# Kernel tuning notes

Hardware: AMD Instinct MI355X
Metric: run time of the kernel (lower is better)

## Reference

```python
import jax, jax.numpy as jnp
import numpy as np

N_NODES = 100_000
N_EDGES = 1_600_000
IN_FEAT = 128
N_HEADS = 8
OUT_FEAT = 16
HF = N_HEADS * OUT_FEAT  # 128
NEG_SLOPE = 0.2


def setup_inputs() -> dict:
    key = jax.random.key(0)
    k = jax.random.split(key, 9)
    x = jax.random.normal(k[0], (N_NODES, IN_FEAT), dtype=jnp.float32)
    src = jax.random.randint(k[1], (N_EDGES,), 0, N_NODES, dtype=jnp.int64)
    dst = jax.random.randint(k[2], (N_EDGES,), 0, N_NODES, dtype=jnp.int64)
    sv = 1.0 / np.sqrt(IN_FEAT)
    sa = 1.0 / np.sqrt(HF)
    Wv = jax.random.normal(k[3], (IN_FEAT, HF), dtype=jnp.float32) * sv
    bv = jnp.zeros((HF,), dtype=jnp.float32)
    Wq = jax.random.normal(k[4], (HF, N_HEADS), dtype=jnp.float32) * sa
    bq = jnp.zeros((N_HEADS,), dtype=jnp.float32)
    Wk = jax.random.normal(k[5], (HF, N_HEADS), dtype=jnp.float32) * sa
    bk = jnp.zeros((N_HEADS,), dtype=jnp.float32)
    return {"x": x, "src": src, "dst": dst, "Wv": Wv, "bv": bv,
            "Wq": Wq, "bq": bq, "Wk": Wk, "bk": bk}


def reference(x, src, dst, Wv, bv, Wq, bq, Wk, bk):
    # Dense projections (homogeneous graph: h_src == h_dst == h)
    h = x @ Wv + bv                       # [N, H*F]
    q = h @ Wq + bq                       # [N, H]  (query, attached via dst)
    k = h @ Wk + bk                       # [N, H]  (key, attached via src)
    u = h.reshape(N_NODES, N_HEADS, OUT_FEAT)  # [N, H, F]

    # Edge scores: u_add_v('k','q') -> e_ij = k[src] + q[dst], then leaky-relu
    e = k[src] + q[dst]                   # [E, H]
    coeff = jnp.where(e >= 0, e, NEG_SLOPE * e)

    # Segment softmax over incoming edges of each destination node
    seg_max = jax.ops.segment_max(coeff, dst, num_segments=N_NODES)   # [N, H]
    ex = jnp.exp(coeff - seg_max[dst])                                # [E, H]
    denom = jax.ops.segment_sum(ex, dst, num_segments=N_NODES)       # [N, H]
    attn = ex / denom[dst]                                           # [E, H]

    # Weighted message + scatter-sum aggregate
    m = u[src] * attn[:, :, None]                                    # [E, H, F]
    v = jax.ops.segment_sum(m, dst, num_segments=N_NODES)            # [N, H, F]

    return jnp.mean(v, axis=1)                                       # [N, F]
```

## Files before the change

kernel.cpp:

```cpp
#include <hip/hip_runtime.h>
#include <hip/hip_fp16.h>

#define NFEAT 128
#define NHEADS 8
#define OUTF 16
#define NPB 256
#define MAXNB 512
#define CAP 4736

typedef _Float16 half8 __attribute__((ext_vector_type(8)));
typedef float float4v __attribute__((ext_vector_type(4)));

__global__ __launch_bounds__(256) void prep_kernel(
    const float* __restrict__ Wv, const float* __restrict__ bv,
    const float* __restrict__ Wq, const float* __restrict__ bq,
    const float* __restrict__ Wk, const float* __restrict__ bk,
    float* __restrict__ Wvq, float* __restrict__ Wvk,
    float* __restrict__ bq2, float* __restrict__ bk2, int* __restrict__ tail)
{
    const int t = threadIdx.x;
    const int idx = blockIdx.x * 256 + t;
    if (idx < MAXNB) tail[idx] = 0;
    const int m  = idx >> 10;
    const int j  = (idx >> 3) & 127;
    const int hd = idx & 7;
    const float* w = m ? Wk : Wq;
    float acc = 0.f;
#pragma unroll 8
    for (int c = 0; c < NFEAT; c++) acc += Wv[j * NFEAT + c] * w[c * NHEADS + hd];
    if (m) Wvk[j * NHEADS + hd] = acc;
    else   Wvq[j * NHEADS + hd] = acc;

    if (blockIdx.x == 0 && t < 16) {
        int mm = t >> 3, hh = t & 7;
        const float* ww = mm ? Wk : Wq;
        float a = mm ? bk[hh] : bq[hh];
        for (int c = 0; c < NFEAT; c++) a += bv[c] * ww[c * NHEADS + hh];
        if (mm) bk2[hh] = a;
        else    bq2[hh] = a;
    }
}

__global__ __launch_bounds__(256) void k1_kernel(
    const float* __restrict__ x, const float* __restrict__ Wv,
    const float* __restrict__ bv, const float* __restrict__ Wvq,
    const float* __restrict__ Wvk, const float* __restrict__ bq2,
    const float* __restrict__ bk2, __half* __restrict__ h,
    float* __restrict__ qarr, float* __restrict__ karr, int M,
    const int* __restrict__ src, const int* __restrict__ dst,
    int* __restrict__ tail, int* __restrict__ bin, int E, int NB,
    int GB, int BB)
{
    __shared__ char smem[144 * 136 * 2];
    const int bid = blockIdx.x;
    const int t = threadIdx.x;

    if ((bid & 1) == 0) {
        const int gb = bid >> 1;
        if (gb >= GB) return;
        _Float16 (*sw)[136] = (_Float16(*)[136])smem;

        for (int i = t; i < 128 * 128; i += 256) {
            int k = i >> 7, n = i & 127;
            sw[n][k] = (_Float16)Wv[i];
        }
        for (int i = t; i < 128 * 16; i += 256) {
            int k = i >> 4, o = i & 15;
            float v = (o < 8) ? Wvq[k * 8 + o] : Wvk[k * 8 + (o - 8)];
            sw[128 + o][k] = (_Float16)v;
        }
        __syncthreads();

        const int wave = t >> 6, lane = t & 63;
        const int quad = lane >> 4, l16 = lane & 15;
        const int nstrips = (M + 15) >> 4;

        float bvv[8];
#pragma unroll
        for (int tl = 0; tl < 8; tl++) bvv[tl] = bv[tl * 16 + l16];
        const float qb = (l16 < 8) ? bq2[l16] : bk2[l16 - 8];

#pragma unroll
        for (int s = 0; s < 4; s++) {
            const int strip = gb * 16 + wave * 4 + s;
            if (strip >= nstrips) break;
            const int row0 = strip * 16;
            const int xr = row0 + l16;
            const bool ok = (xr < M);
            const float* xp = x + (size_t)xr * NFEAT + quad * 8;

            half8 af[4];
#pragma unroll
            for (int kc = 0; kc < 4; kc++) {
                float4 f0 = make_float4(0.f, 0.f, 0.f, 0.f);
                float4 f1 = make_float4(0.f, 0.f, 0.f, 0.f);
                if (ok) {
                    f0 = *(const float4*)(xp + kc * 32);
                    f1 = *(const float4*)(xp + kc * 32 + 4);
                }
                half8 a;
                a[0] = (_Float16)f0.x; a[1] = (_Float16)f0.y;
                a[2] = (_Float16)f0.z; a[3] = (_Float16)f0.w;
                a[4] = (_Float16)f1.x; a[5] = (_Float16)f1.y;
                a[6] = (_Float16)f1.z; a[7] = (_Float16)f1.w;
                af[kc] = a;
            }

            float4v acc[9];
#pragma unroll
            for (int tl = 0; tl < 9; tl++) acc[tl] = (float4v){0.f, 0.f, 0.f, 0.f};

#pragma unroll
            for (int kc = 0; kc < 4; kc++) {
#pragma unroll
                for (int tl = 0; tl < 9; tl++) {
                    half8 b = *(const half8*)&sw[tl * 16 + l16][kc * 32 + quad * 8];
                    acc[tl] = __builtin_amdgcn_mfma_f32_16x16x32_f16(af[kc], b, acc[tl], 0, 0, 0);
                }
            }

#pragma unroll
            for (int r = 0; r < 4; r++) {
                int row = row0 + quad * 4 + r;
                if (row < M) {
#pragma unroll
                    for (int tl = 0; tl < 8; tl++)
                        h[(size_t)row * NFEAT + tl * 16 + l16] =
                            __float2half(acc[tl][r] + bvv[tl]);
                    float qv = acc[8][r] + qb;
                    if (l16 < 8) qarr[(size_t)row * NHEADS + l16] = qv;
                    else         karr[(size_t)row * NHEADS + (l16 - 8)] = qv;
                }
            }
        }
    } else {
        const int bb = bid >> 1;
        if (bb >= BB) return;
        int* lcnt  = (int*)smem;
        int* lbase = lcnt + MAXNB;
        const int e0 = bb * 4096;

        for (int i = t; i < MAXNB; i += 256) lcnt[i] = 0;
        __syncthreads();

        int pack[16], bkt[16], rank[16];
#pragma unroll
        for (int k = 0; k < 16; k++) {
            int e = e0 + k * 256 + t;
            bkt[k] = -1;
            if (e < E) {
                int d = dst[e];
                pack[k] = (src[e] << 8) | (d & (NPB - 1));
                bkt[k]  = d >> 8;
                rank[k] = atomicAdd(&lcnt[bkt[k]], 1);
            }
        }
        __syncthreads();
        for (int i = t; i < NB; i += 256)
            lbase[i] = lcnt[i] ? atomicAdd(&tail[i], lcnt[i]) : 0;
        __syncthreads();

#pragma unroll
        for (int k = 0; k < 16; k++) {
            if (bkt[k] >= 0) {
                int pos = lbase[bkt[k]] + rank[k];
                if (pos < CAP) bin[(size_t)bkt[k] * CAP + pos] = pack[k];
            }
        }
    }
}

__global__ __launch_bounds__(512) void bucket_build_kernel(
    const int* __restrict__ bin, const int* __restrict__ tail,
    int* __restrict__ deg, int* __restrict__ off,
    int* __restrict__ csr, int N, int NB)
{
    __shared__ int stail[MAXNB];
    __shared__ int lcnt[NPB];
    __shared__ int lcur[NPB];
    __shared__ int lcsr[CAP];

    const int b = blockIdx.x;
    const int t = threadIdx.x;

    stail[t] = (t < NB) ? tail[t] : 0;
    if (t < NPB) lcnt[t] = 0;
    __syncthreads();

    for (int o = 1; o < MAXNB; o <<= 1) {
        int u = (t >= o) ? stail[t - o] : 0;
        __syncthreads();
        stail[t] += u;
        __syncthreads();
    }
    const int gbase = (b > 0) ? stail[b - 1] : 0;
    const int cnt = min(stail[b] - gbase, CAP);
    const int n0 = b << 8;
    const int* mybin = bin + (size_t)b * CAP;

    for (int i = t; i < cnt; i += 512) atomicAdd(&lcnt[mybin[i] & (NPB - 1)], 1);
    __syncthreads();

    if (t < NPB) lcur[t] = lcnt[t];
    __syncthreads();
    for (int o = 1; o < NPB; o <<= 1) {
        int u = (t < NPB && t >= o) ? lcur[t - o] : 0;
        __syncthreads();
        if (t < NPB) lcur[t] += u;
        __syncthreads();
    }
    if (t < NPB) {
        int excl = lcur[t] - lcnt[t];
        lcur[t] = excl;
        int node = n0 + t;
        if (node < N) {
            deg[node] = lcnt[t];
            off[node] = gbase + excl;
        }
    }
    __syncthreads();

    for (int i = t; i < cnt; i += 512) {
        int p = mybin[i];
        int r = atomicAdd(&lcur[p & (NPB - 1)], 1);
        lcsr[r] = p >> 8;
    }
    __syncthreads();

    for (int i = t; i < cnt; i += 512) csr[gbase + i] = lcsr[i];
}

__global__ __launch_bounds__(256) void agg_kernel(
    const int* __restrict__ csr, const int* __restrict__ off,
    const int* __restrict__ deg, const float* __restrict__ karr,
    const float* __restrict__ qarr, const __half* __restrict__ h,
    float* __restrict__ out, int nnodes)
{
    const int wave = threadIdx.x >> 6;
    const int lane = threadIdx.x & 63;
    const int d = blockIdx.x * 4 + wave;
    if (d >= nnodes) return;

    const int dg = deg[d];
    const int o0 = off[d];
    const int h8  = lane & 7;
    const int eg  = lane >> 4;
    const int l16 = lane & 15;
    const int hd  = l16 >> 1;
    const float q1 = qarr[d * NHEADS + h8];
    const __half* hbase = h + l16 * 8;

    __half2 acc0 = __float2half2_rn(0.f);
    __half2 acc1 = __float2half2_rn(0.f);
    __half2 acc2 = __float2half2_rn(0.f);
    __half2 acc3 = __float2half2_rn(0.f);
    float den8 = 0.f;

    for (int c0 = 0; c0 < dg; c0 += 64) {
        const int cnt = min(64, dg - c0);
        int sv = (lane < cnt) ? csr[o0 + c0 + lane] : 0;
        for (int g0 = 0; g0 < cnt; g0 += 8) {
            const int epos = g0 + (lane >> 3);
            int s8 = __shfl(sv, epos, 64);
            float p = 0.f;
            if (epos < cnt) {
                float c = karr[s8 * NHEADS + h8] + q1;
                c = fmaxf(c, 0.2f * c);
                p = __expf(c) * 0.0009765625f;
            }
            den8 += p;
            __half2 ph2 = __half2half2(__float2half(p));
            int phi = *(int*)&ph2;
#pragma unroll
            for (int i = 0; i < 2; ++i) {
                int jr  = (i << 2) + eg;
                int sl  = __shfl(sv, g0 + jr, 64);
                int pw  = __shfl(phi, (jr << 3) + hd, 64);
                __half2 pv = *(__half2*)&pw;
                float4 raw = *(const float4*)(hbase + (size_t)sl * NFEAT);
                __half2 v0 = *(__half2*)&raw.x;
                __half2 v1 = *(__half2*)&raw.y;
                __half2 v2 = *(__half2*)&raw.z;
                __half2 v3 = *(__half2*)&raw.w;
                acc0 = __hfma2(pv, v0, acc0);
                acc1 = __hfma2(pv, v1, acc1);
                acc2 = __hfma2(pv, v2, acc2);
                acc3 = __hfma2(pv, v3, acc3);
            }
        }
    }

    den8 += __shfl_xor(den8, 8, 64);
    den8 += __shfl_xor(den8, 16, 64);
    den8 += __shfl_xor(den8, 32, 64);
    float dh = __shfl(den8, hd, 64);

    float f[8];
    f[0] = __low2float(acc0); f[1] = __high2float(acc0);
    f[2] = __low2float(acc1); f[3] = __high2float(acc1);
    f[4] = __low2float(acc2); f[5] = __high2float(acc2);
    f[6] = __low2float(acc3); f[7] = __high2float(acc3);

#pragma unroll
    for (int o = 16; o <= 32; o <<= 1)
#pragma unroll
        for (int i = 0; i < 8; i++) f[i] += __shfl_xor(f[i], o, 64);

    const float inv = (dg > 0) ? 0.125f / dh : 0.f;
#pragma unroll
    for (int i = 0; i < 8; i++) f[i] *= inv;

#pragma unroll
    for (int o = 2; o <= 8; o <<= 1)
#pragma unroll
        for (int i = 0; i < 8; i++) f[i] += __shfl_xor(f[i], o, 64);

    if (lane < 2) {
        float4* o4 = (float4*)(out + (size_t)d * OUTF + lane * 8);
        o4[0] = make_float4(f[0], f[1], f[2], f[3]);
        o4[1] = make_float4(f[4], f[5], f[6], f[7]);
    }
}

extern "C" void kernel_launch(void* const* d_in, const int* in_sizes, int n_in,
                              void* d_out, int out_size, void* d_ws, size_t ws_size,
                              hipStream_t stream)
{
    const float* x   = (const float*)d_in[0];
    const int*   src = (const int*)d_in[1];
    const int*   dst = (const int*)d_in[2];
    const float* Wv  = (const float*)d_in[3];
    const float* bv  = (const float*)d_in[4];
    const float* Wq  = (const float*)d_in[5];
    const float* bq  = (const float*)d_in[6];
    const float* Wk  = (const float*)d_in[7];
    const float* bk  = (const float*)d_in[8];
    float* out = (float*)d_out;

    const int N = in_sizes[0] / NFEAT;
    const int E = in_sizes[1];
    const int NB = (N + NPB - 1) / NPB;

    __half* h   = (__half*)d_ws;
    float* qarr = (float*)d_ws + (size_t)N * (NFEAT / 2);
    float* karr = qarr + (size_t)N * NHEADS;
    int* deg    = (int*)(karr + (size_t)N * NHEADS);
    int* off    = deg + N;
    int* csr    = off + N;
    float* Wvq  = (float*)(csr + E);
    float* Wvk  = Wvq + NFEAT * NHEADS;
    float* bq2  = Wvk + NFEAT * NHEADS;
    float* bk2  = bq2 + NHEADS;
    int* tail   = (int*)(bk2 + NHEADS);
    int* bin    = tail + MAXNB;

    prep_kernel<<<dim3(8), dim3(256), 0, stream>>>(Wv, bv, Wq, bq, Wk, bk,
                                                   Wvq, Wvk, bq2, bk2, tail);

    const int nstrips = (N + 15) / 16;
    const int GB = (nstrips + 15) / 16;
    const int BB = (E + 4095) / 4096;
    const int grid1 = 2 * max(GB, BB);
    k1_kernel<<<dim3(grid1), dim3(256), 0, stream>>>(
        x, Wv, bv, Wvq, Wvk, bq2, bk2, h, qarr, karr, N,
        src, dst, tail, bin, E, NB, GB, BB);

    bucket_build_kernel<<<dim3(NB), dim3(512), 0, stream>>>(
        bin, tail, deg, off, csr, N, NB);

    agg_kernel<<<dim3((N + 3) / 4), dim3(256), 0, stream>>>(
        csr, off, deg, karr, qarr, h, out, N);
}
```

Baseline: 242.9 us.

## Fuse CSR bucket build into aggregation and restructure projection GEMM per-wave

Merges the bucket-build and aggregation kernels so each block sorts its bucket of edges into shared memory and aggregates its 128 destination nodes directly. This drops the global CSR, degree and offset arrays and one launch. Buckets shrink to 128 nodes with a smaller cap. The projection GEMM now keeps each wave's weight column slice in registers, with 9 waves per 576-thread block streaming 18 strips through shared memory. The fused kernel has only 8 waves per bucket, which risks load imbalance and lower occupancy in aggregation, and the cap risks silently dropping edges if a bucket overflows.

```diff
diff --git a/kernel.cpp b/kernel.cpp
--- a/kernel.cpp
+++ b/kernel.cpp
@@ -4,9 +4,10 @@
 #define NFEAT 128
 #define NHEADS 8
 #define OUTF 16
-#define NPB 256
-#define MAXNB 512
-#define CAP 4736
+#define NPB 128
+#define MAXNB 1024
+#define CAP 2816
+#define SPB 18
 
 typedef _Float16 half8 __attribute__((ext_vector_type(8)));
 typedef float float4v __attribute__((ext_vector_type(4)));
@@ -41,7 +42,7 @@
     }
 }
 
-__global__ __launch_bounds__(256) void k1_kernel(
+__global__ __launch_bounds__(576) void k1_kernel(
     const float* __restrict__ x, const float* __restrict__ Wv,
     const float* __restrict__ bv, const float* __restrict__ Wvq,
     const float* __restrict__ Wvk, const float* __restrict__ bq2,
@@ -51,117 +52,113 @@
     int* __restrict__ tail, int* __restrict__ bin, int E, int NB,
     int GB, int BB)
 {
-    __shared__ char smem[144 * 136 * 2];
+    __shared__ alignas(16) int smem4[2048];
     const int bid = blockIdx.x;
     const int t = threadIdx.x;
 
     if ((bid & 1) == 0) {
         const int gb = bid >> 1;
         if (gb >= GB) return;
-        _Float16 (*sw)[136] = (_Float16(*)[136])smem;
-
-        for (int i = t; i < 128 * 128; i += 256) {
-            int k = i >> 7, n = i & 127;
-            sw[n][k] = (_Float16)Wv[i];
-        }
-        for (int i = t; i < 128 * 16; i += 256) {
-            int k = i >> 4, o = i & 15;
-            float v = (o < 8) ? Wvq[k * 8 + o] : Wvk[k * 8 + (o - 8)];
-            sw[128 + o][k] = (_Float16)v;
-        }
-        __syncthreads();
-
-        const int wave = t >> 6, lane = t & 63;
+        _Float16 (*sa)[136] = (_Float16(*)[136])smem4;
+
+        const int wave = t / 64, lane = t & 63;
         const int quad = lane >> 4, l16 = lane & 15;
         const int nstrips = (M + 15) >> 4;
 
-        float bvv[8];
-#pragma unroll
-        for (int tl = 0; tl < 8; tl++) bvv[tl] = bv[tl * 16 + l16];
-        const float qb = (l16 < 8) ? bq2[l16] : bk2[l16 - 8];
-
-#pragma unroll
-        for (int s = 0; s < 4; s++) {
-            const int strip = gb * 16 + wave * 4 + s;
+        half8 bf[4];
+        float bias;
+        if (wave < 8) {
+            const int n = wave * 16 + l16;
+#pragma unroll
+            for (int kc = 0; kc < 4; kc++) {
+                half8 b;
+#pragma unroll
+                for (int j = 0; j < 8; j++)
+                    b[j] = (_Float16)Wv[(kc * 32 + quad * 8 + j) * NFEAT + n];
+                bf[kc] = b;
+            }
+            bias = bv[wave * 16 + l16];
+        } else {
+            const int o = l16;
+#pragma unroll
+            for (int kc = 0; kc < 4; kc++) {
+                half8 b;
+#pragma unroll
+                for (int j = 0; j < 8; j++) {
+                    int k = kc * 32 + quad * 8 + j;
+                    b[j] = (_Float16)((o < 8) ? Wvq[k * 8 + o] : Wvk[k * 8 + (o - 8)]);
+                }
+                bf[kc] = b;
+            }
+            bias = (o < 8) ? bq2[o] : bk2[o - 8];
+        }
+
+        for (int s = 0; s < SPB; s++) {
+            const int strip = gb * SPB + s;
             if (strip >= nstrips) break;
             const int row0 = strip * 16;
-            const int xr = row0 + l16;
-            const bool ok = (xr < M);
-            const float* xp = x + (size_t)xr * NFEAT + quad * 8;
-
-            half8 af[4];
+
+            __syncthreads();
+            if (t < 512) {
+                int r = t >> 5, c4 = (t & 31) << 2;
+                int row = row0 + r;
+                float4 v = make_float4(0.f, 0.f, 0.f, 0.f);
+                if (row < M) v = *(const float4*)&x[(size_t)row * NFEAT + c4];
+                sa[r][c4 + 0] = (_Float16)v.x; sa[r][c4 + 1] = (_Float16)v.y;
+                sa[r][c4 + 2] = (_Float16)v.z; sa[r][c4 + 3] = (_Float16)v.w;
+            }
+            __syncthreads();
+
+            float4v acc = (float4v){0.f, 0.f, 0.f, 0.f};
 #pragma unroll
             for (int kc = 0; kc < 4; kc++) {
-                float4 f0 = make_float4(0.f, 0.f, 0.f, 0.f);
-                float4 f1 = make_float4(0.f, 0.f, 0.f, 0.f);
-                if (ok) {
-                    f0 = *(const float4*)(xp + kc * 32);
-                    f1 = *(const float4*)(xp + kc * 32 + 4);
-                }
-                half8 a;
-                a[0] = (_Float16)f0.x; a[1] = (_Float16)f0.y;
-                a[2] = (_Float16)f0.z; a[3] = (_Float16)f0.w;
-                a[4] = (_Float16)f1.x; a[5] = (_Float16)f1.y;
-                a[6] = (_Float16)f1.z; a[7] = (_Float16)f1.w;
-                af[kc] = a;
-            }
-
-            float4v acc[9];
-#pragma unroll
-            for (int tl = 0; tl < 9; tl++) acc[tl] = (float4v){0.f, 0.f, 0.f, 0.f};
-
-#pragma unroll
-            for (int kc = 0; kc < 4; kc++) {
-#pragma unroll
-                for (int tl = 0; tl < 9; tl++) {
-                    half8 b = *(const half8*)&sw[tl * 16 + l16][kc * 32 + quad * 8];
-                    acc[tl] = __builtin_amdgcn_mfma_f32_16x16x32_f16(af[kc], b, acc[tl], 0, 0, 0);
-                }
+                half8 a = *(const half8*)&sa[l16][kc * 32 + quad * 8];
+                acc = __builtin_amdgcn_mfma_f32_16x16x32_f16(a, bf[kc], acc, 0, 0, 0);
             }
 
 #pragma unroll
             for (int r = 0; r < 4; r++) {
                 int row = row0 + quad * 4 + r;
                 if (row < M) {
-#pragma unroll
-                    for (int tl = 0; tl < 8; tl++)
-                        h[(size_t)row * NFEAT + tl * 16 + l16] =
-                            __float2half(acc[tl][r] + bvv[tl]);
-                    float qv = acc[8][r] + qb;
-                    if (l16 < 8) qarr[(size_t)row * NHEADS + l16] = qv;
-                    else         karr[(size_t)row * NHEADS + (l16 - 8)] = qv;
+                    float v = acc[r] + bias;
+                    if (wave < 8)
+                        h[(size_t)row * NFEAT + wave * 16 + l16] = __float2half(v);
+                    else if (l16 < 8)
+                        qarr[(size_t)row * NHEADS + l16] = v;
+                    else
+                        karr[(size_t)row * NHEADS + (l16 - 8)] = v;
                 }
             }
         }
     } else {
         const int bb = bid >> 1;
         if (bb >= BB) return;
-        int* lcnt  = (int*)smem;
-        int* lbase = lcnt + MAXNB;
-        const int e0 = bb * 4096;
-
-        for (int i = t; i < MAXNB; i += 256) lcnt[i] = 0;
-        __syncthreads();
-
-        int pack[16], bkt[16], rank[16];
-#pragma unroll
-        for (int k = 0; k < 16; k++) {
-            int e = e0 + k * 256 + t;
+        int* lcnt  = smem4;
+        int* lbase = smem4 + MAXNB;
+        const int e0 = bb * 4608;
+
+        for (int i = t; i < MAXNB; i += 576) lcnt[i] = 0;
+        __syncthreads();
+
+        int pack[8], bkt[8], rank[8];
+#pragma unroll
+        for (int k = 0; k < 8; k++) {
+            int e = e0 + k * 576 + t;
             bkt[k] = -1;
             if (e < E) {
                 int d = dst[e];
-                pack[k] = (src[e] << 8) | (d & (NPB - 1));
-                bkt[k]  = d >> 8;
+                pack[k] = (src[e] << 7) | (d & (NPB - 1));
+                bkt[k]  = d >> 7;
                 rank[k] = atomicAdd(&lcnt[bkt[k]], 1);
             }
         }
         __syncthreads();
-        for (int i = t; i < NB; i += 256)
+        for (int i = t; i < NB; i += 576)
             lbase[i] = lcnt[i] ? atomicAdd(&tail[i], lcnt[i]) : 0;
         __syncthreads();
 
 #pragma unroll
-        for (int k = 0; k < 16; k++) {
+        for (int k = 0; k < 8; k++) {
             if (bkt[k] >= 0) {
                 int pos = lbase[bkt[k]] + rank[k];
                 if (pos < CAP) bin[(size_t)bkt[k] * CAP + pos] = pack[k];
@@ -170,33 +167,24 @@
     }
 }
 
-__global__ __launch_bounds__(512) void bucket_build_kernel(
+__global__ __launch_bounds__(512) void buildagg_kernel(
     const int* __restrict__ bin, const int* __restrict__ tail,
-    int* __restrict__ deg, int* __restrict__ off,
-    int* __restrict__ csr, int N, int NB)
+    const float* __restrict__ karr, const float* __restrict__ qarr,
+    const __half* __restrict__ h, float* __restrict__ out, int N)
 {
-    __shared__ int stail[MAXNB];
     __shared__ int lcnt[NPB];
+    __shared__ int loff[NPB];
     __shared__ int lcur[NPB];
     __shared__ int lcsr[CAP];
 
     const int b = blockIdx.x;
     const int t = threadIdx.x;
-
-    stail[t] = (t < NB) ? tail[t] : 0;
+    const int cnt = min(tail[b], CAP);
+    const int n0 = b << 7;
+    const int* mybin = bin + (size_t)b * CAP;
+
     if (t < NPB) lcnt[t] = 0;
     __syncthreads();
-
-    for (int o = 1; o < MAXNB; o <<= 1) {
-        int u = (t >= o) ? stail[t - o] : 0;
-        __syncthreads();
-        stail[t] += u;
-        __syncthreads();
-    }
-    const int gbase = (b > 0) ? stail[b - 1] : 0;
-    const int cnt = min(stail[b] - gbase, CAP);
-    const int n0 = b << 8;
-    const int* mybin = bin + (size_t)b * CAP;
 
     for (int i = t; i < cnt; i += 512) atomicAdd(&lcnt[mybin[i] & (NPB - 1)], 1);
     __syncthreads();
@@ -210,115 +198,100 @@
         __syncthreads();
     }
     if (t < NPB) {
-        int excl = lcur[t] - lcnt[t];
-        lcur[t] = excl;
-        int node = n0 + t;
-        if (node < N) {
-            deg[node] = lcnt[t];
-            off[node] = gbase + excl;
-        }
+        int e = lcur[t] - lcnt[t];
+        loff[t] = e;
+        lcur[t] = e;
     }
     __syncthreads();
 
     for (int i = t; i < cnt; i += 512) {
         int p = mybin[i];
         int r = atomicAdd(&lcur[p & (NPB - 1)], 1);
-        lcsr[r] = p >> 8;
-    }
-    __syncthreads();
-
-    for (int i = t; i < cnt; i += 512) csr[gbase + i] = lcsr[i];
-}
-
-__global__ __launch_bounds__(256) void agg_kernel(
-    const int* __restrict__ csr, const int* __restrict__ off,
-    const int* __restrict__ deg, const float* __restrict__ karr,
-    const float* __restrict__ qarr, const __half* __restrict__ h,
-    float* __restrict__ out, int nnodes)
-{
-    const int wave = threadIdx.x >> 6;
-    const int lane = threadIdx.x & 63;
-    const int d = blockIdx.x * 4 + wave;
-    if (d >= nnodes) return;
-
-    const int dg = deg[d];
-    const int o0 = off[d];
+        lcsr[r] = p >> 7;
+    }
+    __syncthreads();
+
+    const int wave = t >> 6, lane = t & 63;
     const int h8  = lane & 7;
     const int eg  = lane >> 4;
     const int l16 = lane & 15;
     const int hd  = l16 >> 1;
-    const float q1 = qarr[d * NHEADS + h8];
     const __half* hbase = h + l16 * 8;
 
-    __half2 acc0 = __float2half2_rn(0.f);
-    __half2 acc1 = __float2half2_rn(0.f);
-    __half2 acc2 = __float2half2_rn(0.f);
-    __half2 acc3 = __float2half2_rn(0.f);
-    float den8 = 0.f;
-
-    for (int c0 = 0; c0 < dg; c0 += 64) {
-        const int cnt = min(64, dg - c0);
-        int sv = (lane < cnt) ? csr[o0 + c0 + lane] : 0;
-        for (int g0 = 0; g0 < cnt; g0 += 8) {
-            const int epos = g0 + (lane >> 3);
-            int s8 = __shfl(sv, epos, 64);
-            float p = 0.f;
-            if (epos < cnt) {
-                float c = karr[s8 * NHEADS + h8] + q1;
-                c = fmaxf(c, 0.2f * c);
-                p = __expf(c) * 0.0009765625f;
-            }
-            den8 += p;
-            __half2 ph2 = __half2half2(__float2half(p));
-            int phi = *(int*)&ph2;
-#pragma unroll
-            for (int i = 0; i < 2; ++i) {
-                int jr  = (i << 2) + eg;
-                int sl  = __shfl(sv, g0 + jr, 64);
-                int pw  = __shfl(phi, (jr << 3) + hd, 64);
-                __half2 pv = *(__half2*)&pw;
-                float4 raw = *(const float4*)(hbase + (size_t)sl * NFEAT);
-                __half2 v0 = *(__half2*)&raw.x;
-                __half2 v1 = *(__half2*)&raw.y;
-                __half2 v2 = *(__half2*)&raw.z;
-                __half2 v3 = *(__half2*)&raw.w;
-                acc0 = __hfma2(pv, v0, acc0);
-                acc1 = __hfma2(pv, v1, acc1);
-                acc2 = __hfma2(pv, v2, acc2);
-                acc3 = __hfma2(pv, v3, acc3);
-            }
-        }
-    }
-
-    den8 += __shfl_xor(den8, 8, 64);
-    den8 += __shfl_xor(den8, 16, 64);
-    den8 += __shfl_xor(den8, 32, 64);
-    float dh = __shfl(den8, hd, 64);
-
-    float f[8];
-    f[0] = __low2float(acc0); f[1] = __high2float(acc0);
-    f[2] = __low2float(acc1); f[3] = __high2float(acc1);
-    f[4] = __low2float(acc2); f[5] = __high2float(acc2);
-    f[6] = __low2float(acc3); f[7] = __high2float(acc3);
-
-#pragma unroll
-    for (int o = 16; o <= 32; o <<= 1)
-#pragma unroll
-        for (int i = 0; i < 8; i++) f[i] += __shfl_xor(f[i], o, 64);
-
-    const float inv = (dg > 0) ? 0.125f / dh : 0.f;
-#pragma unroll
-    for (int i = 0; i < 8; i++) f[i] *= inv;
-
-#pragma unroll
-    for (int o = 2; o <= 8; o <<= 1)
-#pragma unroll
-        for (int i = 0; i < 8; i++) f[i] += __shfl_xor(f[i], o, 64);
-
-    if (lane < 2) {
-        float4* o4 = (float4*)(out + (size_t)d * OUTF + lane * 8);
-        o4[0] = make_float4(f[0], f[1], f[2], f[3]);
-        o4[1] = make_float4(f[4], f[5], f[6], f[7]);
+    for (int i = 0; i < 16; i++) {
+        const int ln = wave * 16 + i;
+        const int node = n0 + ln;
+        if (node >= N) break;
+        const int dg = lcnt[ln];
+        const int o0 = loff[ln];
+        const float q1 = qarr[node * NHEADS + h8];
+
+        __half2 acc0 = __float2half2_rn(0.f);
+        __half2 acc1 = __float2half2_rn(0.f);
+        __half2 acc2 = __float2half2_rn(0.f);
+        __half2 acc3 = __float2half2_rn(0.f);
+        float den8 = 0.f;
+
+        for (int c0 = 0; c0 < dg; c0 += 64) {
+            const int cnt2 = min(64, dg - c0);
+            int sv = (lane < cnt2) ? lcsr[o0 + c0 + lane] : 0;
+            for (int g0 = 0; g0 < cnt2; g0 += 8) {
+                const int epos = g0 + (lane >> 3);
+                int s8 = __shfl(sv, epos, 64);
+                float p = 0.f;
+                if (epos < cnt2) {
+                    float c = karr[s8 * NHEADS + h8] + q1;
+                    c = fmaxf(c, 0.2f * c);
+                    p = __expf(c) * 0.0009765625f;
+                }
+                den8 += p;
+                __half2 ph2 = __half2half2(__float2half(p));
+                int phi = *(int*)&ph2;
+#pragma unroll
+                for (int u = 0; u < 2; ++u) {
+                    int jr  = (u << 2) + eg;
+                    int sl  = __shfl(sv, g0 + jr, 64);
+                    int pw  = __shfl(phi, (jr << 3) + hd, 64);
+                    __half2 pv = *(__half2*)&pw;
+                    float4 raw = *(const float4*)(hbase + (size_t)sl * NFEAT);
+                    acc0 = __hfma2(pv, *(__half2*)&raw.x, acc0);
+                    acc1 = __hfma2(pv, *(__half2*)&raw.y, acc1);
+                    acc2 = __hfma2(pv, *(__half2*)&raw.z, acc2);
+                    acc3 = __hfma2(pv, *(__half2*)&raw.w, acc3);
+                }
+            }
+        }
+
+        den8 += __shfl_xor(den8, 8, 64);
+        den8 += __shfl_xor(den8, 16, 64);
+        den8 += __shfl_xor(den8, 32, 64);
+        float dh = __shfl(den8, hd, 64);
+
+        float f[8];
+        f[0] = __low2float(acc0); f[1] = __high2float(acc0);
+        f[2] = __low2float(acc1); f[3] = __high2float(acc1);
+        f[4] = __low2float(acc2); f[5] = __high2float(acc2);
+        f[6] = __low2float(acc3); f[7] = __high2float(acc3);
+
+#pragma unroll
+        for (int o = 16; o <= 32; o <<= 1)
+#pragma unroll
+            for (int j = 0; j < 8; j++) f[j] += __shfl_xor(f[j], o, 64);
+
+        const float inv = (dg > 0) ? 0.125f / dh : 0.f;
+#pragma unroll
+        for (int j = 0; j < 8; j++) f[j] *= inv;
+
+#pragma unroll
+        for (int o = 2; o <= 8; o <<= 1)
+#pragma unroll
+            for (int j = 0; j < 8; j++) f[j] += __shfl_xor(f[j], o, 64);
+
+        if (lane < 2) {
+            float4* o4 = (float4*)(out + (size_t)node * OUTF + lane * 8);
+            o4[0] = make_float4(f[0], f[1], f[2], f[3]);
+            o4[1] = make_float4(f[4], f[5], f[6], f[7]);
+        }
     }
 }
 
@@ -344,10 +317,7 @@
     __half* h   = (__half*)d_ws;
     float* qarr = (float*)d_ws + (size_t)N * (NFEAT / 2);
     float* karr = qarr + (size_t)N * NHEADS;
-    int* deg    = (int*)(karr + (size_t)N * NHEADS);
-    int* off    = deg + N;
-    int* csr    = off + N;
-    float* Wvq  = (float*)(csr + E);
+    float* Wvq  = karr + (size_t)N * NHEADS;
     float* Wvk  = Wvq + NFEAT * NHEADS;
     float* bq2  = Wvk + NFEAT * NHEADS;
     float* bk2  = bq2 + NHEADS;
@@ -358,16 +328,13 @@
                                                    Wvq, Wvk, bq2, bk2, tail);
 
     const int nstrips = (N + 15) / 16;
-    const int GB = (nstrips + 15) / 16;
-    const int BB = (E + 4095) / 4096;
+    const int GB = (nstrips + SPB - 1) / SPB;
+    const int BB = (E + 4607) / 4608;
     const int grid1 = 2 * max(GB, BB);
-    k1_kernel<<<dim3(grid1), dim3(256), 0, stream>>>(
+    k1_kernel<<<dim3(grid1), dim3(576), 0, stream>>>(
         x, Wv, bv, Wvq, Wvk, bq2, bk2, h, qarr, karr, N,
         src, dst, tail, bin, E, NB, GB, BB);
 
-    bucket_build_kernel<<<dim3(NB), dim3(512), 0, stream>>>(
-        bin, tail, deg, off, csr, N, NB);
-
-    agg_kernel<<<dim3((N + 3) / 4), dim3(256), 0, stream>>>(
-        csr, off, deg, karr, qarr, h, out, N);
+    buildagg_kernel<<<dim3(NB), dim3(512), 0, stream>>>(
+        bin, tail, karr, qarr, h, out, N);
 }
```

Result: slower. 267.0 us (+9.9%).

## Reschedule pipeline: fuse edge binning with weight prep, GEMM with CSR build

Applied to the files above, without the earlier changes.

The four-kernel pipeline is rearranged. Edge binning now runs in the first kernel alongside weight packing, which writes a pre-transposed fp16 weight tile (Wv plus the folded Wv·Wq/Wv·Wk columns) to global memory. The node projection GEMM then runs in the same launch as the bucket CSR build. Each GEMM block now copies the packed tile with vector loads instead of converting and transposing Wv itself, and blocks grow to 512 threads with fewer strips per wave. This drops one kernel launch and one serialization point. The cost is a memset call and a larger shared-memory footprint shared by both roles.

```diff
diff --git a/kernel.cpp b/kernel.cpp
--- a/kernel.cpp
+++ b/kernel.cpp
@@ -7,67 +7,114 @@
 #define NPB 256
 #define MAXNB 512
 #define CAP 4736
+#define PACKN 144
+#define PACKP 136
 
 typedef _Float16 half8 __attribute__((ext_vector_type(8)));
 typedef float float4v __attribute__((ext_vector_type(4)));
 
-__global__ __launch_bounds__(256) void prep_kernel(
+__global__ __launch_bounds__(512) void u1_kernel(
+    const int* __restrict__ src, const int* __restrict__ dst,
+    int* __restrict__ tail, int* __restrict__ bin, int E, int NB,
     const float* __restrict__ Wv, const float* __restrict__ bv,
     const float* __restrict__ Wq, const float* __restrict__ bq,
     const float* __restrict__ Wk, const float* __restrict__ bk,
-    float* __restrict__ Wvq, float* __restrict__ Wvk,
-    float* __restrict__ bq2, float* __restrict__ bk2, int* __restrict__ tail)
+    __half* __restrict__ pack, float* __restrict__ bq2, float* __restrict__ bk2,
+    int BB)
 {
+    __shared__ int lcnt[MAXNB];
+    __shared__ int lbase[MAXNB];
+    const int bid = blockIdx.x;
     const int t = threadIdx.x;
-    const int idx = blockIdx.x * 256 + t;
-    if (idx < MAXNB) tail[idx] = 0;
-    const int m  = idx >> 10;
-    const int j  = (idx >> 3) & 127;
-    const int hd = idx & 7;
-    const float* w = m ? Wk : Wq;
-    float acc = 0.f;
+
+    if ((bid & 1) == 0) {
+        const int bb = bid >> 1;
+        if (bb >= BB) return;
+        const int e0 = bb * 4096;
+
+        for (int i = t; i < MAXNB; i += 512) lcnt[i] = 0;
+        __syncthreads();
+
+        int pk[8], bkt[8], rank[8];
+#pragma unroll
+        for (int k = 0; k < 8; k++) {
+            int e = e0 + k * 512 + t;
+            bkt[k] = -1;
+            if (e < E) {
+                int d = dst[e];
+                pk[k]  = (src[e] << 8) | (d & (NPB - 1));
+                bkt[k] = d >> 8;
+                rank[k] = atomicAdd(&lcnt[bkt[k]], 1);
+            }
+        }
+        __syncthreads();
+        for (int i = t; i < NB; i += 512)
+            lbase[i] = lcnt[i] ? atomicAdd(&tail[i], lcnt[i]) : 0;
+        __syncthreads();
+
+#pragma unroll
+        for (int k = 0; k < 8; k++) {
+            if (bkt[k] >= 0) {
+                int pos = lbase[bkt[k]] + rank[k];
+                if (pos < CAP) bin[(size_t)bkt[k] * CAP + pos] = pk[k];
+            }
+        }
+    } else {
+        const int pid = bid >> 1;
+        if (pid >= 8) return;
+        if (pid < 4) {
+            const int idx = pid * 512 + t;
+            const int m  = idx >> 10;
+            const int j  = (idx >> 3) & 127;
+            const int hd = idx & 7;
+            const float* w = m ? Wk : Wq;
+            float acc = 0.f;
 #pragma unroll 8
-    for (int c = 0; c < NFEAT; c++) acc += Wv[j * NFEAT + c] * w[c * NHEADS + hd];
-    if (m) Wvk[j * NHEADS + hd] = acc;
-    else   Wvq[j * NHEADS + hd] = acc;
-
-    if (blockIdx.x == 0 && t < 16) {
-        int mm = t >> 3, hh = t & 7;
-        const float* ww = mm ? Wk : Wq;
-        float a = mm ? bk[hh] : bq[hh];
-        for (int c = 0; c < NFEAT; c++) a += bv[c] * ww[c * NHEADS + hh];
-        if (mm) bk2[hh] = a;
-        else    bq2[hh] = a;
+            for (int c = 0; c < NFEAT; c++) acc += Wv[j * NFEAT + c] * w[c * NHEADS + hd];
+            pack[(size_t)(128 + m * 8 + hd) * PACKP + j] = __float2half(acc);
+
+            if (pid == 0 && t < 16) {
+                int mm = t >> 3, hh = t & 7;
+                const float* ww = mm ? Wk : Wq;
+                float a = mm ? bk[hh] : bq[hh];
+                for (int c = 0; c < NFEAT; c++) a += bv[c] * ww[c * NHEADS + hh];
+                if (mm) bk2[hh] = a;
+                else    bq2[hh] = a;
+            }
+        } else {
+            const int idx = (pid - 4) * 512 + t;
+            const int n  = idx >> 4;
+            const int k0 = (idx & 15) * 8;
+            half8 v;
+#pragma unroll
+            for (int j = 0; j < 8; j++) v[j] = (_Float16)Wv[(k0 + j) * NFEAT + n];
+            *(half8*)&pack[(size_t)n * PACKP + k0] = v;
+        }
     }
 }
 
-__global__ __launch_bounds__(256) void k1_kernel(
-    const float* __restrict__ x, const float* __restrict__ Wv,
-    const float* __restrict__ bv, const float* __restrict__ Wvq,
-    const float* __restrict__ Wvk, const float* __restrict__ bq2,
+__global__ __launch_bounds__(512) void u2_kernel(
+    const float* __restrict__ x, const __half* __restrict__ pack,
+    const float* __restrict__ bv, const float* __restrict__ bq2,
     const float* __restrict__ bk2, __half* __restrict__ h,
-    float* __restrict__ qarr, float* __restrict__ karr, int M,
-    const int* __restrict__ src, const int* __restrict__ dst,
-    int* __restrict__ tail, int* __restrict__ bin, int E, int NB,
-    int GB, int BB)
+    float* __restrict__ qarr, float* __restrict__ karr, int M, int GB,
+    const int* __restrict__ bin, const int* __restrict__ tail,
+    int* __restrict__ deg, int* __restrict__ off, int* __restrict__ csr,
+    int N, int NB)
 {
-    __shared__ char smem[144 * 136 * 2];
+    __shared__ alignas(16) char smem[PACKN * PACKP * 2];
     const int bid = blockIdx.x;
     const int t = threadIdx.x;
 
     if ((bid & 1) == 0) {
         const int gb = bid >> 1;
         if (gb >= GB) return;
-        _Float16 (*sw)[136] = (_Float16(*)[136])smem;
-
-        for (int i = t; i < 128 * 128; i += 256) {
-            int k = i >> 7, n = i & 127;
-            sw[n][k] = (_Float16)Wv[i];
-        }
-        for (int i = t; i < 128 * 16; i += 256) {
-            int k = i >> 4, o = i & 15;
-            float v = (o < 8) ? Wvq[k * 8 + o] : Wvk[k * 8 + (o - 8)];
-            sw[128 + o][k] = (_Float16)v;
+        _Float16 (*sw)[PACKP] = (_Float16(*)[PACKP])smem;
+
+        {
+            const float4* gp = (const float4*)pack;
+            float4* sp = (float4*)smem;
+            for (int i = t; i < (PACKN * PACKP * 2) / 16; i += 512) sp[i] = gp[i];
         }
         __syncthreads();
 
@@ -81,8 +128,8 @@
         const float qb = (l16 < 8) ? bq2[l16] : bk2[l16 - 8];
 
 #pragma unroll
-        for (int s = 0; s < 4; s++) {
-            const int strip = gb * 16 + wave * 4 + s;
+        for (int s = 0; s < 2; s++) {
+            const int strip = gb * 16 + wave * 2 + s;
             if (strip >= nstrips) break;
             const int row0 = strip * 16;
             const int xr = row0 + l16;
@@ -134,100 +181,59 @@
             }
         }
     } else {
-        const int bb = bid >> 1;
-        if (bb >= BB) return;
-        int* lcnt  = (int*)smem;
-        int* lbase = lcnt + MAXNB;
-        const int e0 = bb * 4096;
-
-        for (int i = t; i < MAXNB; i += 256) lcnt[i] = 0;
-        __syncthreads();
-
-        int pack[16], bkt[16], rank[16];
-#pragma unroll
-        for (int k = 0; k < 16; k++) {
-            int e = e0 + k * 256 + t;
-            bkt[k] = -1;
-            if (e < E) {
-                int d = dst[e];
-                pack[k] = (src[e] << 8) | (d & (NPB - 1));
-                bkt[k]  = d >> 8;
-                rank[k] = atomicAdd(&lcnt[bkt[k]], 1);
-            }
-        }
-        __syncthreads();
-        for (int i = t; i < NB; i += 256)
-            lbase[i] = lcnt[i] ? atomicAdd(&tail[i], lcnt[i]) : 0;
-        __syncthreads();
-
-#pragma unroll
-        for (int k = 0; k < 16; k++) {
-            if (bkt[k] >= 0) {
-                int pos = lbase[bkt[k]] + rank[k];
-                if (pos < CAP) bin[(size_t)bkt[k] * CAP + pos] = pack[k];
-            }
-        }
+        const int b = bid >> 1;
+        if (b >= NB) return;
+        int* stail = (int*)smem;
+        int* lcnt  = stail + MAXNB;
+        int* lcur  = lcnt + NPB;
+        int* lcsr  = lcur + NPB;
+
+        stail[t] = (t < NB) ? tail[t] : 0;
+        if (t < NPB) lcnt[t] = 0;
+        __syncthreads();
+
+        for (int o = 1; o < MAXNB; o <<= 1) {
+            int u = (t >= o) ? stail[t - o] : 0;
+            __syncthreads();
+            stail[t] += u;
+            __syncthreads();
+        }
+        const int gbase = (b > 0) ? stail[b - 1] : 0;
+        const int cnt = min(stail[b] - gbase, CAP);
+        const int n0 = b << 8;
+        const int* mybin = bin + (size_t)b * CAP;
+
+        for (int i = t; i < cnt; i += 512) atomicAdd(&lcnt[mybin[i] & (NPB - 1)], 1);
+        __syncthreads();
+
+        if (t < NPB) lcur[t] = lcnt[t];
+        __syncthreads();
+        for (int o = 1; o < NPB; o <<= 1) {
+            int u = (t < NPB && t >= o) ? lcur[t - o] : 0;
+            __syncthreads();
+            if (t < NPB) lcur[t] += u;
+            __syncthreads();
+        }
+        if (t < NPB) {
+            int excl = lcur[t] - lcnt[t];
+            lcur[t] = excl;
+            int node = n0 + t;
+            if (node < N) {
+                deg[node] = lcnt[t];
+                off[node] = gbase + excl;
+            }
+        }
+        __syncthreads();
+
+        for (int i = t; i < cnt; i += 512) {
+            int p = mybin[i];
+            int r = atomicAdd(&lcur[p & (NPB - 1)], 1);
+            lcsr[r] = p >> 8;
+        }
+        __syncthreads();
+
+        for (int i = t; i < cnt; i += 512) csr[gbase + i] = lcsr[i];
     }
-}
-
-__global__ __launch_bounds__(512) void bucket_build_kernel(
-    const int* __restrict__ bin, const int* __restrict__ tail,
-    int* __restrict__ deg, int* __restrict__ off,
-    int* __restrict__ csr, int N, int NB)
-{
-    __shared__ int stail[MAXNB];
-    __shared__ int lcnt[NPB];
-    __shared__ int lcur[NPB];
-    __shared__ int lcsr[CAP];
-
-    const int b = blockIdx.x;
-    const int t = threadIdx.x;
-
-    stail[t] = (t < NB) ? tail[t] : 0;
-    if (t < NPB) lcnt[t] = 0;
-    __syncthreads();
-
-    for (int o = 1; o < MAXNB; o <<= 1) {
-        int u = (t >= o) ? stail[t - o] : 0;
-        __syncthreads();
-        stail[t] += u;
-        __syncthreads();
-    }
-    const int gbase = (b > 0) ? stail[b - 1] : 0;
-    const int cnt = min(stail[b] - gbase, CAP);
-    const int n0 = b << 8;
-    const int* mybin = bin + (size_t)b * CAP;
-
-    for (int i = t; i < cnt; i += 512) atomicAdd(&lcnt[mybin[i] & (NPB - 1)], 1);
-    __syncthreads();
-
-    if (t < NPB) lcur[t] = lcnt[t];
-    __syncthreads();
-    for (int o = 1; o < NPB; o <<= 1) {
-        int u = (t < NPB && t >= o) ? lcur[t - o] : 0;
-        __syncthreads();
-        if (t < NPB) lcur[t] += u;
-        __syncthreads();
-    }
-    if (t < NPB) {
-        int excl = lcur[t] - lcnt[t];
-        lcur[t] = excl;
-        int node = n0 + t;
-        if (node < N) {
-            deg[node] = lcnt[t];
-            off[node] = gbase + excl;
-        }
-    }
-    __syncthreads();
-
-    for (int i = t; i < cnt; i += 512) {
-        int p = mybin[i];
-        int r = atomicAdd(&lcur[p & (NPB - 1)], 1);
-        lcsr[r] = p >> 8;
-    }
-    __syncthreads();
-
-    for (int i = t; i < cnt; i += 512) csr[gbase + i] = lcsr[i];
 }
 
 __global__ __launch_bounds__(256) void agg_kernel(
@@ -278,14 +284,10 @@
                 int pw  = __shfl(phi, (jr << 3) + hd, 64);
                 __half2 pv = *(__half2*)&pw;
                 float4 raw = *(const float4*)(hbase + (size_t)sl * NFEAT);
-                __half2 v0 = *(__half2*)&raw.x;
-                __half2 v1 = *(__half2*)&raw.y;
-                __half2 v2 = *(__half2*)&raw.z;
-                __half2 v3 = *(__half2*)&raw.w;
-                acc0 = __hfma2(pv, v0, acc0);
-                acc1 = __hfma2(pv, v1, acc1);
-                acc2 = __hfma2(pv, v2, acc2);
-                acc3 = __hfma2(pv, v3, acc3);
+                acc0 = __hfma2(pv, *(__half2*)&raw.x, acc0);
+                acc1 = __hfma2(pv, *(__half2*)&raw.y, acc1);
+                acc2 = __hfma2(pv, *(__half2*)&raw.z, acc2);
+                acc3 = __hfma2(pv, *(__half2*)&raw.w, acc3);
             }
         }
     }
@@ -347,25 +349,23 @@
     int* deg    = (int*)(karr + (size_t)N * NHEADS);
     int* off    = deg + N;
     int* csr    = off + N;
-    float* Wvq  = (float*)(csr + E);
-    float* Wvk  = Wvq + NFEAT * NHEADS;
-    float* bq2  = Wvk + NFEAT * NHEADS;
+    float* bq2  = (float*)(csr + E);
     float* bk2  = bq2 + NHEADS;
-    int* tail   = (int*)(bk2 + NHEADS);
+    __half* pack = (__half*)(bk2 + NHEADS);
+    int* tail   = (int*)pack + (PACKN * PACKP) / 2;
     int* bin    = tail + MAXNB;
 
-    prep_kernel<<<dim3(8), dim3(256), 0, stream>>>(Wv, bv, Wq, bq, Wk, bk,
-                                                   Wvq, Wvk, bq2, bk2, tail);
+    hipMemsetAsync(tail, 0, MAXNB * sizeof(int), stream);
+
+    const int BB = (E + 4095) / 4096;
+    u1_kernel<<<dim3(2 * BB), dim3(512), 0, stream>>>(
+        src, dst, tail, bin, E, NB,
+        Wv, bv, Wq, bq, Wk, bk, pack, bq2, bk2, BB);
 
     const int nstrips = (N + 15) / 16;
     const int GB = (nstrips + 15) / 16;
-    const int BB = (E + 4095) / 4096;
-    const int grid1 = 2 * max(GB, BB);
-    k1_kernel<<<dim3(grid1), dim3(256), 0, stream>>>(
-        x, Wv, bv, Wvq, Wvk, bq2, bk2, h, qarr, karr, N,
-        src, dst, tail, bin, E, NB, GB, BB);
-
-    bucket_build_kernel<<<dim3(NB), dim3(512), 0, stream>>>(
+    u2_kernel<<<dim3(2 * ((GB > NB) ? GB : NB)), dim3(512), 0, stream>>>(
+        x, pack, bv, bq2, bk2, h, qarr, karr, N, GB,
         bin, tail, deg, off, csr, N, NB);
 
     agg_kernel<<<dim3((N + 3) / 4), dim3(256), 0, stream>>>(
```

New measurement: 240.1 us. Within noise of the previous version (-1.2%).
